# Optimization experiments

Hardware: AMD Instinct MI355X
Metric: run time of the kernel (lower is better)

## Reference

```python
import jax, jax.numpy as jnp
import numpy as np

D = 1024
H = 16
DH = D // H


def setup_inputs() -> dict:
    key = jax.random.key(0)
    ks = jax.random.split(key, 9)
    s = 1.0 / np.sqrt(D)
    return {
        "x": jax.random.normal(ks[0], (4, 2048, D), dtype=jnp.float32),
        "wq": jax.random.uniform(ks[1], (D, D), jnp.float32, -s, s),
        "bq": jax.random.uniform(ks[2], (D,), jnp.float32, -s, s),
        "wk": jax.random.uniform(ks[3], (D, D), jnp.float32, -s, s),
        "bk": jax.random.uniform(ks[4], (D,), jnp.float32, -s, s),
        "wv": jax.random.uniform(ks[5], (D, D), jnp.float32, -s, s),
        "bv": jax.random.uniform(ks[6], (D,), jnp.float32, -s, s),
        "wo": jax.random.uniform(ks[7], (D, D), jnp.float32, -s, s),
        "bo": jax.random.uniform(ks[8], (D,), jnp.float32, -s, s),
    }


def reference(x, wq, bq, wk, bk, wv, bv, wo, bo):
    B, S, _ = x.shape
    # projections + split heads: [B, S, D] -> [B, H, S, Dh]
    def split(t):
        return t.reshape(B, S, H, DH).transpose(0, 2, 1, 3)
    q = split(x @ wq + bq)
    k = split(x @ wk + bk)
    v = split(x @ wv + bv)
    scale = 1.0 / jnp.sqrt(jnp.float32(DH))
    scores = jnp.einsum("bhqd,bhkd->bhqk", q, k) * scale  # [B,H,S,S]
    att = jax.nn.softmax(scores, axis=-1)
    out = jnp.einsum("bhqk,bhkd->bhqd", att, v)  # [B,H,S,Dh]
    out = out.transpose(0, 2, 1, 3).reshape(B, S, D)
    return out @ wo + bo
```

## Files before the change

### kernel.cpp

```cpp
#include <hip/hip_runtime.h>
#include <stdint.h>

typedef float f32x4 __attribute__((ext_vector_type(4)));
typedef __bf16 bf16x8 __attribute__((ext_vector_type(8)));
typedef unsigned short ushort_t;
typedef ushort_t ushortx8 __attribute__((ext_vector_type(8)));
typedef ushort_t ushortx4 __attribute__((ext_vector_type(4)));

#define DEV static __device__ __forceinline__

DEV ushort_t f2bf(float f) {
  union { float f; uint32_t u; } v; v.f = f;
  uint32_t u = v.u;
  return (ushort_t)((u + 0x7FFFu + ((u >> 16) & 1u)) >> 16);
}

DEV uint32_t pkbf(float a, float b) {
  __bf16 x = (__bf16)a, y = (__bf16)b;
  return (uint32_t)__builtin_bit_cast(unsigned short, x) |
         ((uint32_t)__builtin_bit_cast(unsigned short, y) << 16);
}

DEV void cp16(const void* g, void* l) {
  __builtin_amdgcn_global_load_lds((const __attribute__((address_space(1))) unsigned int*)g,
                                   (__attribute__((address_space(3))) unsigned int*)l,
                                   16, 0, 0);
}

DEV f32x4 mfma16(bf16x8 a, bf16x8 b, f32x4 c) {
  return __builtin_amdgcn_mfma_f32_16x16x32_bf16(a, b, c, 0, 0, 0);
}

__global__ __launch_bounds__(256) void k_prep(
    const float* __restrict__ x, ushort_t* __restrict__ xb,
    const float* __restrict__ wq, const float* __restrict__ wk,
    const float* __restrict__ wv, const float* __restrict__ wo,
    ushort_t* __restrict__ wqkvT, ushort_t* __restrict__ woT) {
  __shared__ float tile[32][33];
  int b = blockIdx.x;
  if (b < 4096) {
    size_t idx = ((size_t)b * 256 + threadIdx.x) * 8;
    const float4* src = (const float4*)(x + idx);
    float4 a = src[0], c = src[1];
    ushortx8 o;
    o[0] = f2bf(a.x); o[1] = f2bf(a.y); o[2] = f2bf(a.z); o[3] = f2bf(a.w);
    o[4] = f2bf(c.x); o[5] = f2bf(c.y); o[6] = f2bf(c.z); o[7] = f2bf(c.w);
    *(ushortx8*)(xb + idx) = o;
  } else {
    int t = b - 4096;
    int which = t >> 10;
    const float* src = (which == 0) ? wq : (which == 1) ? wk : (which == 2) ? wv : wo;
    ushort_t* dst = (which == 0) ? wqkvT
                    : (which == 1) ? wqkvT + 1024 * 1024
                    : (which == 2) ? wqkvT + 2 * 1024 * 1024
                                   : woT;
    int tt = t & 1023;
    int c0 = (tt & 31) * 32, r0 = (tt >> 5) * 32;
    int tx = threadIdx.x & 31, ty = threadIdx.x >> 5;
#pragma unroll
    for (int i = ty; i < 32; i += 8)
      tile[i][tx] = src[(size_t)(r0 + i) * 1024 + c0 + tx];
    __syncthreads();
#pragma unroll
    for (int i = ty; i < 32; i += 8)
      dst[(size_t)(c0 + i) * 1024 + r0 + tx] = f2bf(tile[tx][i]);
  }
}

template <int MODE>
__global__ __launch_bounds__(512, 1) void k_gemm2(
    const ushort_t* __restrict__ A, const ushort_t* __restrict__ Bt,
    const float* __restrict__ b0, const float* __restrict__ b1,
    const float* __restrict__ b2, ushort_t* __restrict__ qw,
    ushort_t* __restrict__ kw, ushort_t* __restrict__ vtw,
    float* __restrict__ outf) {
  extern __shared__ ushort_t lds[];
  ushort_t* As2 = lds;
  ushort_t* Bs2 = lds + 2 * 8192;
  const int K = 1024, NT = 16;
  int tid = threadIdx.x;
  int w = tid >> 6, lane = tid & 63, l16 = lane & 15, lg = lane >> 4;
  int wr = w >> 2, wc = w & 3;
  int m0 = blockIdx.x * 128, n0 = blockIdx.y * 256;

  const ushort_t* Asrc = A + (size_t)(m0 + (tid >> 3)) * K +
                         (size_t)(((tid & 7) ^ ((tid >> 3) & 7)) * 8);
  const ushort_t* Bsrc = Bt + (size_t)(n0 + (tid >> 3)) * K +
                         (size_t)(((tid & 7) ^ ((tid >> 3) & 7)) * 8);

  f32x4 acc[4][4] = {};
  bf16x8 a[2][2], b[4][2];
  const int aRow = wr * 64 + l16, bRow = wc * 64 + l16, rsw = l16 & 7;

  cp16(Asrc, As2 + w * 512);
  cp16(Asrc + (size_t)64 * K, As2 + 4096 + w * 512);
#pragma unroll
  for (int s = 0; s < 4; ++s)
    cp16(Bsrc + (size_t)s * 64 * K, Bs2 + s * 4096 + w * 512);
  cp16(Bsrc + 64, Bs2 + 16384 + w * 512);
  cp16(Bsrc + 64 + (size_t)64 * K, Bs2 + 16384 + 4096 + w * 512);
  asm volatile("s_waitcnt vmcnt(2)" ::: "memory");
  __builtin_amdgcn_s_barrier();

  for (int t = 0; t < NT; ++t) {
    int cur = t & 1, nxt = cur ^ 1;
    ushort_t* AsC = As2 + cur * 8192;
    ushort_t* BsC = Bs2 + cur * 16384;
    int t1 = (t + 1 < NT) ? t + 1 : NT - 1;
    int t2 = (t + 2 < NT) ? t + 2 : NT - 1;
    const ushort_t* An = Asrc + (size_t)t1 * 64;
    const ushort_t* Bn = Bsrc + (size_t)t1 * 64;

#pragma unroll
    for (int i2 = 0; i2 < 2; ++i2)
#pragma unroll
      for (int ks = 0; ks < 2; ++ks)
        a[i2][ks] = *(const bf16x8*)&AsC[(aRow + i2 * 16) * 64 +
                                         (((ks << 2) | lg) ^ rsw) * 8];
#pragma unroll
    for (int j2 = 0; j2 < 2; ++j2)
#pragma unroll
      for (int ks = 0; ks < 2; ++ks)
        b[j2][ks] = *(const bf16x8*)&BsC[(bRow + j2 * 16) * 64 +
                                         (((ks << 2) | lg) ^ rsw) * 8];
    cp16(Bn + (size_t)2 * 64 * K, Bs2 + nxt * 16384 + 2 * 4096 + w * 512);
    cp16(Bn + (size_t)3 * 64 * K, Bs2 + nxt * 16384 + 3 * 4096 + w * 512);
    __builtin_amdgcn_s_barrier();
    asm volatile("s_waitcnt lgkmcnt(0)" ::: "memory");
    __builtin_amdgcn_s_setprio(1);
#pragma unroll
    for (int i2 = 0; i2 < 2; ++i2)
#pragma unroll
      for (int j2 = 0; j2 < 2; ++j2)
#pragma unroll
        for (int ks = 0; ks < 2; ++ks)
          acc[i2][j2] = mfma16(a[i2][ks], b[j2][ks], acc[i2][j2]);
    __builtin_amdgcn_s_setprio(0);
    __builtin_amdgcn_s_barrier();

#pragma unroll
    for (int j2 = 2; j2 < 4; ++j2)
#pragma unroll
      for (int ks = 0; ks < 2; ++ks)
        b[j2][ks] = *(const bf16x8*)&BsC[(bRow + j2 * 16) * 64 +
                                         (((ks << 2) | lg) ^ rsw) * 8];
    cp16(An, As2 + nxt * 8192 + w * 512);
    cp16(An + (size_t)64 * K, As2 + nxt * 8192 + 4096 + w * 512);
    __builtin_amdgcn_s_barrier();
    asm volatile("s_waitcnt lgkmcnt(0)" ::: "memory");
    __builtin_amdgcn_s_setprio(1);
#pragma unroll
    for (int i2 = 0; i2 < 2; ++i2)
#pragma unroll
      for (int j2 = 2; j2 < 4; ++j2)
#pragma unroll
        for (int ks = 0; ks < 2; ++ks)
          acc[i2][j2] = mfma16(a[i2][ks], b[j2][ks], acc[i2][j2]);
    __builtin_amdgcn_s_setprio(0);
    __builtin_amdgcn_s_barrier();

#pragma unroll
    for (int i2 = 0; i2 < 2; ++i2)
#pragma unroll
      for (int ks = 0; ks < 2; ++ks)
        a[i2][ks] = *(const bf16x8*)&AsC[(aRow + (2 + i2) * 16) * 64 +
                                         (((ks << 2) | lg) ^ rsw) * 8];
    __builtin_amdgcn_s_barrier();
    asm volatile("s_waitcnt lgkmcnt(0)" ::: "memory");
    __builtin_amdgcn_s_setprio(1);
#pragma unroll
    for (int i2 = 0; i2 < 2; ++i2)
#pragma unroll
      for (int j2 = 2; j2 < 4; ++j2)
#pragma unroll
        for (int ks = 0; ks < 2; ++ks)
          acc[2 + i2][j2] = mfma16(a[i2][ks], b[j2][ks], acc[2 + i2][j2]);
    __builtin_amdgcn_s_setprio(0);
    __builtin_amdgcn_s_barrier();

    cp16(Bsrc + (size_t)t2 * 64, BsC + w * 512);
    cp16(Bsrc + (size_t)t2 * 64 + (size_t)64 * K, BsC + 4096 + w * 512);
    asm volatile("s_waitcnt vmcnt(2)" ::: "memory");
    __builtin_amdgcn_s_barrier();
    __builtin_amdgcn_s_setprio(1);
#pragma unroll
    for (int i2 = 0; i2 < 2; ++i2)
#pragma unroll
      for (int j2 = 0; j2 < 2; ++j2)
#pragma unroll
        for (int ks = 0; ks < 2; ++ks)
          acc[2 + i2][j2] = mfma16(a[i2][ks], b[j2][ks], acc[2 + i2][j2]);
    __builtin_amdgcn_s_setprio(0);
    __builtin_amdgcn_s_barrier();
  }

  if (MODE == 0) {
    const float QSCALE = 0.18033688011112042f;
    int p = blockIdx.x >> 3;
    int cbase = (m0 & 1023) + wr * 64;
    if (p == 2) {
#pragma unroll
      for (int i = 0; i < 4; ++i) {
        int oc = cbase + i * 16 + lg * 4;
        int h = oc >> 6, dh0 = oc & 63;
        float4 bb = *(const float4*)&b2[oc];
#pragma unroll
        for (int j = 0; j < 4; ++j) {
          int tok = n0 + wc * 64 + j * 16 + l16;
          int bi = tok >> 11, tk = tok & 2047;
          size_t vb = ((size_t)((bi * 16 + h) * 64 + dh0)) * 2048 + tk;
          vtw[vb] = f2bf(acc[i][j][0] + bb.x);
          vtw[vb + 2048] = f2bf(acc[i][j][1] + bb.y);
          vtw[vb + 2 * 2048] = f2bf(acc[i][j][2] + bb.z);
          vtw[vb + 3 * 2048] = f2bf(acc[i][j][3] + bb.w);
        }
      }
    } else {
      const float* bias = (p == 0) ? b0 : b1;
      ushort_t* dst = (p == 0) ? qw : kw;
      float qs = (p == 0) ? QSCALE : 1.0f;
#pragma unroll
      for (int i = 0; i < 4; ++i) {
        int oc = cbase + i * 16 + lg * 4;
        int h = oc >> 6, dh0 = oc & 63;
        float4 bb = *(const float4*)&bias[oc];
#pragma unroll
        for (int j = 0; j < 4; ++j) {
          int tok = n0 + wc * 64 + j * 16 + l16;
          size_t base =
              ((size_t)((tok >> 11) * 16 + h) * 2048 + (tok & 2047)) * 64 + dh0;
          ushortx4 pk;
          pk[0] = f2bf((acc[i][j][0] + bb.x) * qs);
          pk[1] = f2bf((acc[i][j][1] + bb.y) * qs);
          pk[2] = f2bf((acc[i][j][2] + bb.z) * qs);
          pk[3] = f2bf((acc[i][j][3] + bb.w) * qs);
          *(ushortx4*)&dst[base] = pk;
        }
      }
    }
  } else {
#pragma unroll
    for (int j = 0; j < 4; ++j) {
      int col = n0 + wc * 64 + j * 16 + l16;
      float bb = b0[col];
#pragma unroll
      for (int i = 0; i < 4; ++i) {
#pragma unroll
        for (int r = 0; r < 4; ++r) {
          int row = m0 + wr * 64 + i * 16 + lg * 4 + r;
          outf[(size_t)row * 1024 + col] = acc[i][j][r] + bb;
        }
      }
    }
  }
}

__global__ __launch_bounds__(512, 2) void k_attn(
    const ushort_t* __restrict__ qg, const ushort_t* __restrict__ kg,
    const ushort_t* __restrict__ vtg, ushort_t* __restrict__ att) {
  __shared__ ushort_t Ks[2][64 * 64];
  __shared__ ushort_t Vs[2][64 * 64];
  __shared__ ushort_t Ps[8][16 * 128];
  int tid = threadIdx.x;
  int w = tid >> 6, lane = tid & 63, l16 = lane & 15, lg = lane >> 4;
  int i = blockIdx.x;
  int bh = (i & 7) * 8 + ((i >> 3) & 7);
  int q0 = (i >> 6) * 256;
  const ushort_t* qh = qg + (size_t)bh * 2048 * 64;

  const ushort_t* kstage = kg + (size_t)bh * 2048 * 64 + (size_t)(tid >> 3) * 64 +
                           (size_t)(((tid & 7) ^ ((tid >> 3) & 7)) * 8);
  const ushort_t* vstage = vtg + (size_t)bh * 64 * 2048 + (size_t)(tid >> 3) * 2048 +
                           (size_t)(((tid & 7) ^ ((tid >> 3) & 7)) * 8);

  bf16x8 qf[2][2];
#pragma unroll
  for (int st = 0; st < 2; ++st)
#pragma unroll
    for (int ks = 0; ks < 2; ++ks)
      qf[st][ks] = *(const bf16x8*)(qh + (size_t)(q0 + w * 32 + st * 16 + l16) * 64 +
                                    ks * 32 + lg * 8);

  bf16x8 vone;
#pragma unroll
  for (int t = 0; t < 8; ++t) vone[t] = (__bf16)1.0f;

  f32x4 o[2][5] = {};

  cp16(kstage, &Ks[0][tid * 8]);
  cp16(vstage, &Vs[0][tid * 8]);
  __syncthreads();

  for (int t = 0; t < 32; ++t) {
    int cur = t & 1, nxt = cur ^ 1;
    cp16(kstage + (size_t)(t + 1) * 64 * 64, &Ks[nxt][tid * 8]);
    cp16(vstage + (size_t)(t + 1) * 64, &Vs[nxt][tid * 8]);

    f32x4 sc[2][4] = {};
    __builtin_amdgcn_s_setprio(1);
#pragma unroll
    for (int jt = 0; jt < 4; ++jt) {
      int row = jt * 16 + l16;
      bf16x8 kf0 = *(const bf16x8*)&Ks[cur][row * 64 + ((lg) ^ (l16 & 7)) * 8];
      bf16x8 kf1 = *(const bf16x8*)&Ks[cur][row * 64 + ((lg + 4) ^ (l16 & 7)) * 8];
      sc[0][jt] = mfma16(kf0, qf[0][0], sc[0][jt]);
      sc[0][jt] = mfma16(kf1, qf[0][1], sc[0][jt]);
      sc[1][jt] = mfma16(kf0, qf[1][0], sc[1][jt]);
      sc[1][jt] = mfma16(kf1, qf[1][1], sc[1][jt]);
    }
    __builtin_amdgcn_s_setprio(0);

#pragma unroll
    for (int st = 0; st < 2; ++st)
#pragma unroll
      for (int jt = 0; jt < 4; ++jt) {
        float e0 = __builtin_amdgcn_exp2f(sc[st][jt][0]);
        float e1 = __builtin_amdgcn_exp2f(sc[st][jt][1]);
        float e2 = __builtin_amdgcn_exp2f(sc[st][jt][2]);
        float e3 = __builtin_amdgcn_exp2f(sc[st][jt][3]);
        uint2 pk2;
        pk2.x = pkbf(e0, e1);
        pk2.y = pkbf(e2, e3);
        *(uint2*)&Ps[w][l16 * 128 +
                        (((st * 8 + jt * 2 + (lg >> 1)) ^ l16) * 8) +
                        (lg & 1) * 4] = pk2;
      }

    __builtin_amdgcn_s_setprio(1);
#pragma unroll
    for (int ks = 0; ks < 2; ++ks) {
      bf16x8 pf0 =
          *(const bf16x8*)&Ps[w][l16 * 128 + (((ks * 4 + lg) ^ l16) * 8)];
      bf16x8 pf1 =
          *(const bf16x8*)&Ps[w][l16 * 128 + (((8 + ks * 4 + lg) ^ l16) * 8)];
      o[0][4] = mfma16(pf0, vone, o[0][4]);
      o[1][4] = mfma16(pf1, vone, o[1][4]);
#pragma unroll
      for (int dt = 0; dt < 4; ++dt) {
        int vrow = dt * 16 + l16;
        bf16x8 vf =
            *(const bf16x8*)&Vs[cur][vrow * 64 + (((ks * 4 + lg) ^ (l16 & 7)) * 8)];
        o[0][dt] = mfma16(pf0, vf, o[0][dt]);
        o[1][dt] = mfma16(pf1, vf, o[1][dt]);
      }
    }
    __builtin_amdgcn_s_setprio(0);

    __syncthreads();
  }

  int bi = bh >> 4, h = bh & 15;
#pragma unroll
  for (int st = 0; st < 2; ++st) {
    f32x4 inv;
#pragma unroll
    for (int r = 0; r < 4; ++r) inv[r] = __builtin_amdgcn_rcpf(o[st][4][r]);
#pragma unroll
    for (int dt = 0; dt < 4; ++dt)
#pragma unroll
      for (int r = 0; r < 4; ++r) {
        int srow = q0 + w * 32 + st * 16 + lg * 4 + r;
        int col = h * 64 + dt * 16 + l16;
        att[(size_t)(bi * 2048 + srow) * 1024 + col] = f2bf(o[st][dt][r] * inv[r]);
      }
  }
}

extern "C" void kernel_launch(void* const* d_in, const int* in_sizes, int n_in,
                              void* d_out, int out_size, void* d_ws, size_t ws_size,
                              hipStream_t stream) {
  const float* x = (const float*)d_in[0];
  const float* wq = (const float*)d_in[1];
  const float* bq = (const float*)d_in[2];
  const float* wk = (const float*)d_in[3];
  const float* bk = (const float*)d_in[4];
  const float* wv = (const float*)d_in[5];
  const float* bv = (const float*)d_in[6];
  const float* wo = (const float*)d_in[7];
  const float* bo = (const float*)d_in[8];
  float* out = (float*)d_out;

  char* ws = (char*)d_ws;
  ushort_t* xb = (ushort_t*)(ws);
  ushort_t* wqkvT = (ushort_t*)(ws + 16777216);
  ushort_t* woT = (ushort_t*)(ws + 23068672);
  ushort_t* qw = (ushort_t*)(ws + 25165824);
  ushort_t* kw = (ushort_t*)(ws + 41943040);
  ushort_t* vtw = (ushort_t*)(ws + 58720256);
  ushort_t* att = (ushort_t*)(ws + 75497472);

  k_prep<<<dim3(8192), dim3(256), 0, stream>>>(x, xb, wq, wk, wv, wo, wqkvT, woT);

  const int G2_LDS = 98304;
  hipFuncSetAttribute(reinterpret_cast<const void*>(&k_gemm2<0>),
                      hipFuncAttributeMaxDynamicSharedMemorySize, G2_LDS);
  hipFuncSetAttribute(reinterpret_cast<const void*>(&k_gemm2<1>),
                      hipFuncAttributeMaxDynamicSharedMemorySize, G2_LDS);

  k_gemm2<0><<<dim3(24, 32), dim3(512), G2_LDS, stream>>>(
      wqkvT, xb, bq, bk, bv, qw, kw, vtw, nullptr);

  k_attn<<<dim3(512), dim3(512), 0, stream>>>(qw, kw, vtw, att);

  k_gemm2<1><<<dim3(64, 4), dim3(512), G2_LDS, stream>>>(
      att, woT, bo, nullptr, nullptr, nullptr, nullptr, nullptr, out);
}
```

Before: 270.4 us.

## Triple-buffer LDS in GEMM to prefetch two K-tiles ahead

Switches the projection GEMM's LDS staging from a double buffer with partial in-place refill to a three-stage ring buffer. Each iteration issues loads for tile t+2 into the free slot, spread across the compute phases, and waits with vmcnt(6) so one full tile of loads stays in flight. The goal is to hide more global-load latency behind MFMA work. In exchange, dynamic LDS grows from 96KB to 144KB per block.

```diff
diff --git a/kernel.cpp b/kernel.cpp
--- a/kernel.cpp
+++ b/kernel.cpp
@@ -75,8 +75,8 @@
     ushort_t* __restrict__ kw, ushort_t* __restrict__ vtw,
     float* __restrict__ outf) {
   extern __shared__ ushort_t lds[];
-  ushort_t* As2 = lds;
-  ushort_t* Bs2 = lds + 2 * 8192;
+  ushort_t* As3 = lds;
+  ushort_t* Bs3 = lds + 3 * 8192;
   const int K = 1024, NT = 16;
   int tid = threadIdx.x;
   int w = tid >> 6, lane = tid & 63, l16 = lane & 15, lg = lane >> 4;
@@ -92,24 +92,27 @@
   bf16x8 a[2][2], b[4][2];
   const int aRow = wr * 64 + l16, bRow = wc * 64 + l16, rsw = l16 & 7;
 
-  cp16(Asrc, As2 + w * 512);
-  cp16(Asrc + (size_t)64 * K, As2 + 4096 + w * 512);
-#pragma unroll
-  for (int s = 0; s < 4; ++s)
-    cp16(Bsrc + (size_t)s * 64 * K, Bs2 + s * 4096 + w * 512);
-  cp16(Bsrc + 64, Bs2 + 16384 + w * 512);
-  cp16(Bsrc + 64 + (size_t)64 * K, Bs2 + 16384 + 4096 + w * 512);
-  asm volatile("s_waitcnt vmcnt(2)" ::: "memory");
+#pragma unroll
+  for (int tt = 0; tt < 2; ++tt) {
+    cp16(Asrc + (size_t)tt * 64, As3 + tt * 8192 + w * 512);
+    cp16(Asrc + (size_t)tt * 64 + (size_t)64 * K, As3 + tt * 8192 + 4096 + w * 512);
+#pragma unroll
+    for (int s = 0; s < 4; ++s)
+      cp16(Bsrc + (size_t)tt * 64 + (size_t)s * 64 * K,
+           Bs3 + tt * 16384 + s * 4096 + w * 512);
+  }
+  asm volatile("s_waitcnt vmcnt(6)" ::: "memory");
   __builtin_amdgcn_s_barrier();
 
+  int cur = 0, nx2 = 2;
   for (int t = 0; t < NT; ++t) {
-    int cur = t & 1, nxt = cur ^ 1;
-    ushort_t* AsC = As2 + cur * 8192;
-    ushort_t* BsC = Bs2 + cur * 16384;
-    int t1 = (t + 1 < NT) ? t + 1 : NT - 1;
+    ushort_t* AsC = As3 + cur * 8192;
+    ushort_t* BsC = Bs3 + cur * 16384;
+    ushort_t* AsN = As3 + nx2 * 8192;
+    ushort_t* BsN = Bs3 + nx2 * 16384;
     int t2 = (t + 2 < NT) ? t + 2 : NT - 1;
-    const ushort_t* An = Asrc + (size_t)t1 * 64;
-    const ushort_t* Bn = Bsrc + (size_t)t1 * 64;
+    const ushort_t* A2 = Asrc + (size_t)t2 * 64;
+    const ushort_t* B2 = Bsrc + (size_t)t2 * 64;
 
 #pragma unroll
     for (int i2 = 0; i2 < 2; ++i2)
@@ -123,8 +126,8 @@
       for (int ks = 0; ks < 2; ++ks)
         b[j2][ks] = *(const bf16x8*)&BsC[(bRow + j2 * 16) * 64 +
                                          (((ks << 2) | lg) ^ rsw) * 8];
-    cp16(Bn + (size_t)2 * 64 * K, Bs2 + nxt * 16384 + 2 * 4096 + w * 512);
-    cp16(Bn + (size_t)3 * 64 * K, Bs2 + nxt * 16384 + 3 * 4096 + w * 512);
+    cp16(A2, AsN + w * 512);
+    cp16(A2 + (size_t)64 * K, AsN + 4096 + w * 512);
     __builtin_amdgcn_s_barrier();
     asm volatile("s_waitcnt lgkmcnt(0)" ::: "memory");
     __builtin_amdgcn_s_setprio(1);
@@ -144,8 +147,8 @@
       for (int ks = 0; ks < 2; ++ks)
         b[j2][ks] = *(const bf16x8*)&BsC[(bRow + j2 * 16) * 64 +
                                          (((ks << 2) | lg) ^ rsw) * 8];
-    cp16(An, As2 + nxt * 8192 + w * 512);
-    cp16(An + (size_t)64 * K, As2 + nxt * 8192 + 4096 + w * 512);
+    cp16(B2, BsN + w * 512);
+    cp16(B2 + (size_t)64 * K, BsN + 4096 + w * 512);
     __builtin_amdgcn_s_barrier();
     asm volatile("s_waitcnt lgkmcnt(0)" ::: "memory");
     __builtin_amdgcn_s_setprio(1);
@@ -165,6 +168,8 @@
       for (int ks = 0; ks < 2; ++ks)
         a[i2][ks] = *(const bf16x8*)&AsC[(aRow + (2 + i2) * 16) * 64 +
                                          (((ks << 2) | lg) ^ rsw) * 8];
+    cp16(B2 + (size_t)2 * 64 * K, BsN + 8192 + w * 512);
+    cp16(B2 + (size_t)3 * 64 * K, BsN + 12288 + w * 512);
     __builtin_amdgcn_s_barrier();
     asm volatile("s_waitcnt lgkmcnt(0)" ::: "memory");
     __builtin_amdgcn_s_setprio(1);
@@ -178,9 +183,7 @@
     __builtin_amdgcn_s_setprio(0);
     __builtin_amdgcn_s_barrier();
 
-    cp16(Bsrc + (size_t)t2 * 64, BsC + w * 512);
-    cp16(Bsrc + (size_t)t2 * 64 + (size_t)64 * K, BsC + 4096 + w * 512);
-    asm volatile("s_waitcnt vmcnt(2)" ::: "memory");
+    asm volatile("s_waitcnt vmcnt(6)" ::: "memory");
     __builtin_amdgcn_s_barrier();
     __builtin_amdgcn_s_setprio(1);
 #pragma unroll
@@ -192,6 +195,9 @@
           acc[2 + i2][j2] = mfma16(a[i2][ks], b[j2][ks], acc[2 + i2][j2]);
     __builtin_amdgcn_s_setprio(0);
     __builtin_amdgcn_s_barrier();
+
+    cur = (cur + 1 == 3) ? 0 : cur + 1;
+    nx2 = (nx2 + 1 == 3) ? 0 : nx2 + 1;
   }
 
   if (MODE == 0) {
@@ -391,7 +397,7 @@
 
   k_prep<<<dim3(8192), dim3(256), 0, stream>>>(x, xb, wq, wk, wv, wo, wqkvT, woT);
 
-  const int G2_LDS = 98304;
+  const int G2_LDS = 147456;
   hipFuncSetAttribute(reinterpret_cast<const void*>(&k_gemm2<0>),
                       hipFuncAttributeMaxDynamicSharedMemorySize, G2_LDS);
   hipFuncSetAttribute(reinterpret_cast<const void*>(&k_gemm2<1>),
```

After: 259.1 us, median of 2. 1.04x faster.
